# Kernel optimization log

Measured on AMD Instinct MI355X. Metric: run time of the kernel, lower is better.

## Reference

```python
import jax, jax.numpy as jnp
import numpy as np

H = 32
DECAY = 0.9


def setup_inputs() -> dict:
    key = jax.random.key(0)
    ks = jax.random.split(key, 6)
    B, T, D = 8, 4096, 1024
    x = jax.random.normal(ks[0], (B, T, D), dtype=jnp.float32)
    s = 1.0 / np.sqrt(D)
    Wv = jax.random.normal(ks[1], (D, D), dtype=jnp.float32) * s
    bv = jax.random.normal(ks[2], (D,), dtype=jnp.float32) * s
    Wo = jax.random.normal(ks[3], (D, D), dtype=jnp.float32) * s
    bo = jax.random.normal(ks[4], (D,), dtype=jnp.float32) * s
    w = jnp.asarray(DECAY ** np.arange(H), dtype=jnp.float32)
    decay_w = w / jnp.sum(w)
    return {"x": x, "Wv": Wv, "bv": bv, "Wo": Wo, "bo": bo, "decay_w": decay_w}


def reference(x, Wv, bv, Wo, bo, decay_w):
    # x: [B, T, D]. Original pads H zeros at front and unfolds windows of size H
    # with stride 1, producing T+1 windows: window t covers x[t-H .. t-1].
    # value_proj is linear and applied to every window copy, so it commutes with
    # the fixed-weight sum: attended = (sum_i w_i * x_window_i) @ Wv^T + bv*sum(w).
    B, T, D = x.shape
    Hlen = decay_w.shape[0]
    x_pad = jnp.pad(x, ((0, 0), (Hlen, 0), (0, 0)))  # [B, T+H, D]
    # Depthwise 1D conv over time with the (shared) decay kernel.
    kernel = jnp.broadcast_to(decay_w[:, None, None], (Hlen, 1, D))  # [W, I=1, O=D]
    s = jax.lax.conv_general_dilated(
        x_pad, kernel, window_strides=(1,), padding="VALID",
        dimension_numbers=("NWC", "WIO", "NWC"), feature_group_count=D,
    )  # [B, T+1, D]
    attended = s @ Wv.T + bv * jnp.sum(decay_w)
    return attended @ Wo.T + bo  # [B, T+1, D]
```

## Files before the change

### kernel.cpp

```cpp
#include <hip/hip_runtime.h>
#include <stdint.h>

#define D_DIM 1024
#define T_DIM 4096
#define B_DIM 8
#define M_REAL (B_DIM * (T_DIM + 1))
#define M_MAIN 32768
#define NWG 512

typedef short short8 __attribute__((ext_vector_type(8)));
typedef float floatx4 __attribute__((ext_vector_type(4)));

typedef const __attribute__((address_space(1))) void* gptr_t;
typedef __attribute__((address_space(3))) void* lptr_t;

__device__ __forceinline__ ushort f2bf(float f) {
  union { float f; uint32_t u; } v; v.f = f;
  uint32_t r = v.u + 0x7FFF + ((v.u >> 16) & 1);
  return (ushort)(r >> 16);
}
__device__ __forceinline__ float bf2f(ushort b) {
  union { uint32_t u; float f; } v; v.u = ((uint32_t)b) << 16; return v.f;
}

#define BARRIER()  asm volatile("s_barrier" ::: "memory")
#define WAIT_VM2() asm volatile("s_waitcnt vmcnt(2)" ::: "memory")
#define WAIT_VM0() asm volatile("s_waitcnt vmcnt(0)" ::: "memory")
#define WAIT_LGKM0() do { asm volatile("s_waitcnt lgkmcnt(0)" ::: "memory"); \
                          __builtin_amdgcn_sched_barrier(0); } while (0)
#define SP1() __builtin_amdgcn_s_setprio(1)
#define SP0() __builtin_amdgcn_s_setprio(0)

__global__ __launch_bounds__(1024) void gemm_w16_kernel(
    const ushort* __restrict__ A, const ushort* __restrict__ Bm,
    float* __restrict__ C, const float* __restrict__ bias)
{
  __shared__ char smem[65536];
  const int tid  = threadIdx.x;
  const int wave = tid >> 6;
  const int lane = tid & 63;
  const int wm = wave >> 2, wn = wave & 3;
  const int l15 = lane & 15, lhi = lane >> 4;

  const int bid = blockIdx.x;
  const int wg  = (bid & 7) * 64 + (bid >> 3);
  const int n0 = (wg & 3) * 256;
  const int m0 = (wg >> 2) * 256;

  const int srow = tid >> 2;
  const int ksw  = ((tid & 3) ^ ((tid >> 3) & 3)) * 8;
  const ushort* Aq = A  + (size_t)(m0 + srow) * D_DIM + ksw;
  const ushort* Bq = Bm + (size_t)(n0 + srow) * D_DIM + ksw;

  const int xorc = (lhi ^ ((l15 >> 1) & 3)) * 16;
  const int aoff = (wm * 64 + l15) * 64 + xorc;
  const int boff = (wn * 64 + l15) * 64 + xorc;

  short8 a[4], b[4];
  floatx4 acc[4][4] = {};

#define STAGE_W(PA, PB, S) do { \
  __builtin_amdgcn_global_load_lds((gptr_t)(PA), \
      (lptr_t)(smem + (S) * 16384 + wave * 1024), 16, 0, 0); \
  __builtin_amdgcn_global_load_lds((gptr_t)(PB), \
      (lptr_t)(smem + 32768 + (S) * 16384 + wave * 1024), 16, 0, 0); \
} while (0)

#define LDAB_W(S) do { \
  _Pragma("unroll") \
  for (int m = 0; m < 4; ++m) \
    a[m] = *(const short8*)(smem + (S) * 16384 + aoff + m * 1024); \
  _Pragma("unroll") \
  for (int n = 0; n < 4; ++n) \
    b[n] = *(const short8*)(smem + 32768 + (S) * 16384 + boff + n * 1024); \
} while (0)

#define MFMA_W() do { \
  _Pragma("unroll") \
  for (int m = 0; m < 4; ++m) \
    _Pragma("unroll") \
    for (int n = 0; n < 4; ++n) \
      acc[m][n] = __builtin_amdgcn_mfma_f32_16x16x32_bf16( \
          a[m], b[n], acc[m][n], 0, 0, 0); \
} while (0)

#define ITER_W(S0, STG, VMW) do { \
  if (STG) { STAGE_W(ApS, BpS, (S0) ^ 1); ApS += 32; BpS += 32; } \
  VMW; \
  BARRIER(); \
  LDAB_W(S0); \
  WAIT_LGKM0(); \
  SP1(); MFMA_W(); SP0(); \
  BARRIER(); \
} while (0)

  STAGE_W(Aq, Bq, 0);
  const ushort* ApS = Aq + 32;
  const ushort* BpS = Bq + 32;

#pragma unroll 1
  for (int it = 0; it < 15; ++it) {
    ITER_W(0, 1, WAIT_VM2());
    ITER_W(1, 1, WAIT_VM2());
  }
  ITER_W(0, 1, WAIT_VM2());
  ITER_W(1, 0, WAIT_VM0());

#pragma unroll
  for (int m = 0; m < 4; ++m)
#pragma unroll
    for (int n = 0; n < 4; ++n) {
      const int gn = n0 + wn * 64 + n * 16 + l15;
      const float bia = bias[gn];
#pragma unroll
      for (int j = 0; j < 4; ++j) {
        const int gm = m0 + wm * 64 + m * 16 + lhi * 4 + j;
        C[(size_t)gm * D_DIM + gn] = acc[m][n][j] + bia;
      }
    }
#undef STAGE_W
#undef LDAB_W
#undef MFMA_W
#undef ITER_W
}

__global__ __launch_bounds__(256) void tail_gemv_kernel(
    const ushort* __restrict__ S, const ushort* __restrict__ Wf,
    const float* __restrict__ cvec, float* __restrict__ out)
{
  const int wavei = threadIdx.x >> 6, lane = threadIdx.x & 63;
  const int c = blockIdx.x * 4 + wavei;
  float acc[8] = {};
  for (int i = 0; i < 16; ++i) {
    const int k = i * 64 + lane;
    const float wv = bf2f(Wf[(size_t)c * D_DIM + k]);
#pragma unroll
    for (int r = 0; r < 8; ++r)
      acc[r] += wv * bf2f(S[(size_t)(M_MAIN + r) * D_DIM + k]);
  }
#pragma unroll
  for (int r = 0; r < 8; ++r) {
#pragma unroll
    for (int off = 32; off; off >>= 1) acc[r] += __shfl_xor(acc[r], off, 64);
  }
  if (lane == 0) {
    const float bia = cvec[c];
#pragma unroll
    for (int r = 0; r < 8; ++r)
      out[(size_t)(M_MAIN + r) * D_DIM + c] = acc[r] + bia;
  }
}

__global__ __launch_bounds__(256) void gemm_bt_kernel(
    const ushort* __restrict__ A, const ushort* __restrict__ Bm,
    ushort* __restrict__ Cb, int K, int N)
{
  __shared__ ushort As[128][64];
  __shared__ ushort Bs[128][64];
  const int tid  = threadIdx.x;
  const int wave = tid >> 6;
  const int lane = tid & 63;
  const int wm = wave >> 1, wn = wave & 1;
  const int n0 = blockIdx.x * 128, m0 = blockIdx.y * 128;
  const int l15 = lane & 15, lhi = lane >> 4;

  floatx4 acc[4][4] = {};

  const int srow = tid >> 3;
  const int sk8  = (tid & 7) * 8;
  const ushort* Ab = A  + (size_t)(m0 + srow) * K + sk8;
  const ushort* Bb = Bm + (size_t)(n0 + srow) * K + sk8;

  for (int k0 = 0; k0 < K; k0 += 64) {
#pragma unroll
    for (int q = 0; q < 4; ++q)
      __builtin_amdgcn_global_load_lds((gptr_t)(Ab + k0 + (size_t)q * 32 * K),
          (lptr_t)((char*)&As[0][0] + (q * 256 + wave * 64) * 16), 16, 0, 0);
#pragma unroll
    for (int q = 0; q < 4; ++q)
      __builtin_amdgcn_global_load_lds((gptr_t)(Bb + k0 + (size_t)q * 32 * K),
          (lptr_t)((char*)&Bs[0][0] + (q * 256 + wave * 64) * 16), 16, 0, 0);
    __syncthreads();

#pragma unroll
    for (int kk = 0; kk < 2; ++kk) {
      short8 af[4], bfrg[4];
#pragma unroll
      for (int i = 0; i < 4; ++i) {
        af[i]   = *(const short8*)(&As[wm * 64 + i * 16 + l15][kk * 32 + lhi * 8]);
        bfrg[i] = *(const short8*)(&Bs[wn * 64 + i * 16 + l15][kk * 32 + lhi * 8]);
      }
#pragma unroll
      for (int mi = 0; mi < 4; ++mi)
#pragma unroll
        for (int ni = 0; ni < 4; ++ni)
          acc[mi][ni] = __builtin_amdgcn_mfma_f32_16x16x32_bf16(
              af[mi], bfrg[ni], acc[mi][ni], 0, 0, 0);
    }
    __syncthreads();
  }

#pragma unroll
  for (int mi = 0; mi < 4; ++mi)
#pragma unroll
    for (int ni = 0; ni < 4; ++ni) {
      const int gn = n0 + wn * 64 + ni * 16 + l15;
#pragma unroll
      for (int j = 0; j < 4; ++j) {
        const int gm = m0 + wm * 64 + mi * 16 + lhi * 4 + j;
        Cb[(size_t)gm * N + gn] = f2bf(acc[mi][ni][j]);
      }
    }
}

#define CTCH 256
__global__ __launch_bounds__(256) void conv_kernel(
    const float* __restrict__ x, const float* __restrict__ dw,
    ushort* __restrict__ S)
{
  const int b   = blockIdx.y;
  const int col = blockIdx.z * 256 + threadIdx.x;
  const int t0  = blockIdx.x * CTCH;

  float w[32];
#pragma unroll
  for (int i = 0; i < 32; ++i) w[i] = dw[i];
  const float rinv = w[0] / w[1];
  const float w31  = w[31];
  const float c0   = -w[0] * rinv;

  const float* xb = x + (size_t)b * T_DIM * D_DIM + col;
  ushort*      Sb = S + (size_t)b * (T_DIM + 1) * D_DIM + col;

  float prev[32], cur[32];
  float s;
  if (blockIdx.x == 0) {
#pragma unroll
    for (int i = 0; i < 32; ++i) prev[i] = 0.f;
    s = 0.f;
    Sb[0] = f2bf(0.f);
  } else {
#pragma unroll
    for (int i = 0; i < 32; ++i) prev[i] = xb[(size_t)(t0 - 32 + i) * D_DIM];
    s = 0.f;
#pragma unroll
    for (int i = 0; i < 32; ++i) s = __builtin_fmaf(w[i], prev[i], s);
  }

#pragma unroll 1
  for (int g = 0; g < 8; g += 2) {
#pragma unroll
    for (int i = 0; i < 32; ++i) cur[i] = xb[(size_t)(t0 + g * 32 + i) * D_DIM];
#pragma unroll
    for (int j = 0; j < 32; ++j) {
      s = __builtin_fmaf(s, rinv, __builtin_fmaf(prev[j], c0, w31 * cur[j]));
      Sb[(size_t)(t0 + g * 32 + 1 + j) * D_DIM] = f2bf(s);
    }
    s = 0.f;
#pragma unroll
    for (int i = 0; i < 32; ++i) s = __builtin_fmaf(w[i], cur[i], s);
#pragma unroll
    for (int i = 0; i < 32; ++i) prev[i] = xb[(size_t)(t0 + (g + 1) * 32 + i) * D_DIM];
#pragma unroll
    for (int j = 0; j < 32; ++j) {
      s = __builtin_fmaf(s, rinv, __builtin_fmaf(cur[j], c0, w31 * prev[j]));
      Sb[(size_t)(t0 + (g + 1) * 32 + 1 + j) * D_DIM] = f2bf(s);
    }
    s = 0.f;
#pragma unroll
    for (int i = 0; i < 32; ++i) s = __builtin_fmaf(w[i], prev[i], s);
  }
}

__global__ __launch_bounds__(256) void prep_kernel(
    const float* __restrict__ Wo, const float* __restrict__ Wv,
    const float* __restrict__ bv, const float* __restrict__ bo,
    const float* __restrict__ dw,
    ushort* __restrict__ WoB, ushort* __restrict__ WvT,
    float* __restrict__ cvec)
{
  __shared__ float tile[32][33];
  const int bid = blockIdx.x;
  const int tid = threadIdx.x;

  if (bid < 1024) {
    const int i = bid * 256 + tid;
    const float4 v = ((const float4*)Wo)[i];
    ushort4 o = make_ushort4(f2bf(v.x), f2bf(v.y), f2bf(v.z), f2bf(v.w));
    *(ushort4*)(WoB + (size_t)i * 4) = o;
  } else if (bid < 2048) {
    const int b2 = bid - 1024;
    const int c0 = (b2 & 31) * 32, r0 = (b2 >> 5) * 32;
    const int tx = tid & 31, ty = tid >> 5;
#pragma unroll
    for (int j = 0; j < 4; ++j)
      tile[ty + j * 8][tx] = Wv[(size_t)(r0 + ty + j * 8) * D_DIM + c0 + tx];
    __syncthreads();
#pragma unroll
    for (int j = 0; j < 4; ++j)
      WvT[(size_t)(c0 + ty + j * 8) * D_DIM + r0 + tx] = f2bf(tile[tx][ty + j * 8]);
  } else {
    const int j    = (bid - 2048) * 4 + (tid >> 6);
    const int lane = tid & 63;
    float sumw = 0.f;
#pragma unroll
    for (int i = 0; i < 32; ++i) sumw += dw[i];
    float s = 0.f;
    for (int k = lane; k < D_DIM; k += 64) s += Wo[(size_t)j * D_DIM + k] * bv[k];
#pragma unroll
    for (int off = 32; off; off >>= 1) s += __shfl_xor(s, off, 64);
    if (lane == 0) cvec[j] = sumw * s + bo[j];
  }
}

extern "C" void kernel_launch(void* const* d_in, const int* in_sizes, int n_in,
                              void* d_out, int out_size, void* d_ws, size_t ws_size,
                              hipStream_t stream) {
  const float* x  = (const float*)d_in[0];
  const float* Wv = (const float*)d_in[1];
  const float* bv = (const float*)d_in[2];
  const float* Wo = (const float*)d_in[3];
  const float* bo = (const float*)d_in[4];
  const float* dw = (const float*)d_in[5];
  float* out = (float*)d_out;

  char* ws = (char*)d_ws;
  ushort* S      = (ushort*)ws;
  ushort* WoB    = (ushort*)(ws + (size_t)M_REAL * D_DIM * 2);
  ushort* WvT    = WoB + (size_t)D_DIM * D_DIM;
  ushort* Wfused = WvT + (size_t)D_DIM * D_DIM;
  float*  cvec   = (float*)(Wfused + (size_t)D_DIM * D_DIM);

  prep_kernel<<<dim3(2304), dim3(256), 0, stream>>>(
      Wo, Wv, bv, bo, dw, WoB, WvT, cvec);

  gemm_bt_kernel<<<dim3(8, 8), dim3(256), 0, stream>>>(
      WoB, WvT, Wfused, D_DIM, D_DIM);

  conv_kernel<<<dim3(T_DIM / CTCH, B_DIM, 4), dim3(256), 0, stream>>>(x, dw, S);

  gemm_w16_kernel<<<dim3(NWG), dim3(1024), 0, stream>>>(S, Wfused, out, cvec);
  tail_gemv_kernel<<<dim3(256), dim3(256), 0, stream>>>(S, Wfused, cvec, out);
}
```

Before: 157.4 us.

## Merge conv with weight-fusion GEMM and tail GEMV into main GEMM launch

The conv kernel and the small Wo·Wv GEMM, which are independent, now run as one launch split by block index, so they can execute concurrently. The tail GEMV for the last 8 rows is folded into the main GEMM launch as 16 extra 1024-thread blocks that each handle 64 output columns. Together this cuts two kernel launches and lets small, underfilled kernels overlap with other work. In exchange the extra tail blocks may finish after the main GEMM tiles, and the conv branch now shares a kernel whose LDS footprint is sized for the GEMM branch.

Measured after the change: 173.7 us. 10.3% more time.

```diff
diff --git a/kernel.cpp b/kernel.cpp
--- a/kernel.cpp
+++ b/kernel.cpp
@@ -37,12 +37,42 @@
 {
   __shared__ char smem[65536];
   const int tid  = threadIdx.x;
+  const int bid  = blockIdx.x;
+
+  if (bid >= NWG) {
+    const int eb = bid - NWG;
+    const int wv = tid >> 6, lane = tid & 63;
+#pragma unroll 1
+    for (int cc = 0; cc < 4; ++cc) {
+      const int c = eb * 64 + wv * 4 + cc;
+      float a8[8] = {};
+      for (int i = 0; i < 16; ++i) {
+        const int k = i * 64 + lane;
+        const float wvv = bf2f(Bm[(size_t)c * D_DIM + k]);
+#pragma unroll
+        for (int r = 0; r < 8; ++r)
+          a8[r] += wvv * bf2f(A[(size_t)(M_MAIN + r) * D_DIM + k]);
+      }
+#pragma unroll
+      for (int r = 0; r < 8; ++r) {
+#pragma unroll
+        for (int off = 32; off; off >>= 1) a8[r] += __shfl_xor(a8[r], off, 64);
+      }
+      if (lane == 0) {
+        const float bia = bias[c];
+#pragma unroll
+        for (int r = 0; r < 8; ++r)
+          C[(size_t)(M_MAIN + r) * D_DIM + c] = a8[r] + bia;
+      }
+    }
+    return;
+  }
+
   const int wave = tid >> 6;
   const int lane = tid & 63;
   const int wm = wave >> 2, wn = wave & 3;
   const int l15 = lane & 15, lhi = lane >> 4;
 
-  const int bid = blockIdx.x;
   const int wg  = (bid & 7) * 64 + (bid >> 3);
   const int n0 = (wg & 3) * 256;
   const int m0 = (wg >> 2) * 256;
@@ -124,61 +154,96 @@
 #undef ITER_W
 }
 
-__global__ __launch_bounds__(256) void tail_gemv_kernel(
-    const ushort* __restrict__ S, const ushort* __restrict__ Wf,
-    const float* __restrict__ cvec, float* __restrict__ out)
-{
-  const int wavei = threadIdx.x >> 6, lane = threadIdx.x & 63;
-  const int c = blockIdx.x * 4 + wavei;
-  float acc[8] = {};
-  for (int i = 0; i < 16; ++i) {
-    const int k = i * 64 + lane;
-    const float wv = bf2f(Wf[(size_t)c * D_DIM + k]);
-#pragma unroll
-    for (int r = 0; r < 8; ++r)
-      acc[r] += wv * bf2f(S[(size_t)(M_MAIN + r) * D_DIM + k]);
-  }
-#pragma unroll
-  for (int r = 0; r < 8; ++r) {
-#pragma unroll
-    for (int off = 32; off; off >>= 1) acc[r] += __shfl_xor(acc[r], off, 64);
-  }
-  if (lane == 0) {
-    const float bia = cvec[c];
-#pragma unroll
-    for (int r = 0; r < 8; ++r)
-      out[(size_t)(M_MAIN + r) * D_DIM + c] = acc[r] + bia;
-  }
-}
-
-__global__ __launch_bounds__(256) void gemm_bt_kernel(
-    const ushort* __restrict__ A, const ushort* __restrict__ Bm,
-    ushort* __restrict__ Cb, int K, int N)
+#define CTCH 256
+__global__ __launch_bounds__(256) void conv_bt_kernel(
+    const float* __restrict__ x, const float* __restrict__ dw,
+    ushort* __restrict__ S,
+    const ushort* __restrict__ WoB, const ushort* __restrict__ WvT,
+    ushort* __restrict__ Wfused)
 {
   __shared__ ushort As[128][64];
   __shared__ ushort Bs[128][64];
-  const int tid  = threadIdx.x;
+  const int bid = blockIdx.x;
+  const int tid = threadIdx.x;
+
+  if (bid < 512) {
+    const int t0  = (bid & 15) * CTCH;
+    const int b   = (bid >> 4) & 7;
+    const int col = (bid >> 7) * 256 + tid;
+
+    float w[32];
+#pragma unroll
+    for (int i = 0; i < 32; ++i) w[i] = dw[i];
+    const float rinv = w[0] / w[1];
+    const float w31  = w[31];
+    const float c0   = -w[0] * rinv;
+
+    const float* xb = x + (size_t)b * T_DIM * D_DIM + col;
+    ushort*      Sb = S + (size_t)b * (T_DIM + 1) * D_DIM + col;
+
+    float prev[32], cur[32];
+    float s;
+    if ((bid & 15) == 0) {
+#pragma unroll
+      for (int i = 0; i < 32; ++i) prev[i] = 0.f;
+      s = 0.f;
+      Sb[0] = f2bf(0.f);
+    } else {
+#pragma unroll
+      for (int i = 0; i < 32; ++i) prev[i] = xb[(size_t)(t0 - 32 + i) * D_DIM];
+      s = 0.f;
+#pragma unroll
+      for (int i = 0; i < 32; ++i) s = __builtin_fmaf(w[i], prev[i], s);
+    }
+
+#pragma unroll 1
+    for (int g = 0; g < 8; g += 2) {
+#pragma unroll
+      for (int i = 0; i < 32; ++i) cur[i] = xb[(size_t)(t0 + g * 32 + i) * D_DIM];
+#pragma unroll
+      for (int j = 0; j < 32; ++j) {
+        s = __builtin_fmaf(s, rinv, __builtin_fmaf(prev[j], c0, w31 * cur[j]));
+        Sb[(size_t)(t0 + g * 32 + 1 + j) * D_DIM] = f2bf(s);
+      }
+      s = 0.f;
+#pragma unroll
+      for (int i = 0; i < 32; ++i) s = __builtin_fmaf(w[i], cur[i], s);
+#pragma unroll
+      for (int i = 0; i < 32; ++i) prev[i] = xb[(size_t)(t0 + (g + 1) * 32 + i) * D_DIM];
+#pragma unroll
+      for (int j = 0; j < 32; ++j) {
+        s = __builtin_fmaf(s, rinv, __builtin_fmaf(cur[j], c0, w31 * prev[j]));
+        Sb[(size_t)(t0 + (g + 1) * 32 + 1 + j) * D_DIM] = f2bf(s);
+      }
+      s = 0.f;
+#pragma unroll
+      for (int i = 0; i < 32; ++i) s = __builtin_fmaf(w[i], prev[i], s);
+    }
+    return;
+  }
+
+  const int bid2 = bid - 512;
   const int wave = tid >> 6;
   const int lane = tid & 63;
   const int wm = wave >> 1, wn = wave & 1;
-  const int n0 = blockIdx.x * 128, m0 = blockIdx.y * 128;
+  const int n0 = (bid2 & 7) * 128, m0 = (bid2 >> 3) * 128;
   const int l15 = lane & 15, lhi = lane >> 4;
 
   floatx4 acc[4][4] = {};
 
   const int srow = tid >> 3;
   const int sk8  = (tid & 7) * 8;
-  const ushort* Ab = A  + (size_t)(m0 + srow) * K + sk8;
-  const ushort* Bb = Bm + (size_t)(n0 + srow) * K + sk8;
-
-  for (int k0 = 0; k0 < K; k0 += 64) {
+  const ushort* Ab = WoB + (size_t)(m0 + srow) * D_DIM + sk8;
+  const ushort* Bb = WvT + (size_t)(n0 + srow) * D_DIM + sk8;
+
+  for (int k0 = 0; k0 < D_DIM; k0 += 64) {
 #pragma unroll
     for (int q = 0; q < 4; ++q)
-      __builtin_amdgcn_global_load_lds((gptr_t)(Ab + k0 + (size_t)q * 32 * K),
+      __builtin_amdgcn_global_load_lds((gptr_t)(Ab + k0 + (size_t)q * 32 * D_DIM),
           (lptr_t)((char*)&As[0][0] + (q * 256 + wave * 64) * 16), 16, 0, 0);
 #pragma unroll
     for (int q = 0; q < 4; ++q)
-      __builtin_amdgcn_global_load_lds((gptr_t)(Bb + k0 + (size_t)q * 32 * K),
+      __builtin_amdgcn_global_load_lds((gptr_t)(Bb + k0 + (size_t)q * 32 * D_DIM),
           (lptr_t)((char*)&Bs[0][0] + (q * 256 + wave * 64) * 16), 16, 0, 0);
     __syncthreads();
 
@@ -208,68 +273,9 @@
 #pragma unroll
       for (int j = 0; j < 4; ++j) {
         const int gm = m0 + wm * 64 + mi * 16 + lhi * 4 + j;
-        Cb[(size_t)gm * N + gn] = f2bf(acc[mi][ni][j]);
-      }
-    }
-}
-
-#define CTCH 256
-__global__ __launch_bounds__(256) void conv_kernel(
-    const float* __restrict__ x, const float* __restrict__ dw,
-    ushort* __restrict__ S)
-{
-  const int b   = blockIdx.y;
-  const int col = blockIdx.z * 256 + threadIdx.x;
-  const int t0  = blockIdx.x * CTCH;
-
-  float w[32];
-#pragma unroll
-  for (int i = 0; i < 32; ++i) w[i] = dw[i];
-  const float rinv = w[0] / w[1];
-  const float w31  = w[31];
-  const float c0   = -w[0] * rinv;
-
-  const float* xb = x + (size_t)b * T_DIM * D_DIM + col;
-  ushort*      Sb = S + (size_t)b * (T_DIM + 1) * D_DIM + col;
-
-  float prev[32], cur[32];
-  float s;
-  if (blockIdx.x == 0) {
-#pragma unroll
-    for (int i = 0; i < 32; ++i) prev[i] = 0.f;
-    s = 0.f;
-    Sb[0] = f2bf(0.f);
-  } else {
-#pragma unroll
-    for (int i = 0; i < 32; ++i) prev[i] = xb[(size_t)(t0 - 32 + i) * D_DIM];
-    s = 0.f;
-#pragma unroll
-    for (int i = 0; i < 32; ++i) s = __builtin_fmaf(w[i], prev[i], s);
-  }
-
-#pragma unroll 1
-  for (int g = 0; g < 8; g += 2) {
-#pragma unroll
-    for (int i = 0; i < 32; ++i) cur[i] = xb[(size_t)(t0 + g * 32 + i) * D_DIM];
-#pragma unroll
-    for (int j = 0; j < 32; ++j) {
-      s = __builtin_fmaf(s, rinv, __builtin_fmaf(prev[j], c0, w31 * cur[j]));
-      Sb[(size_t)(t0 + g * 32 + 1 + j) * D_DIM] = f2bf(s);
-    }
-    s = 0.f;
-#pragma unroll
-    for (int i = 0; i < 32; ++i) s = __builtin_fmaf(w[i], cur[i], s);
-#pragma unroll
-    for (int i = 0; i < 32; ++i) prev[i] = xb[(size_t)(t0 + (g + 1) * 32 + i) * D_DIM];
-#pragma unroll
-    for (int j = 0; j < 32; ++j) {
-      s = __builtin_fmaf(s, rinv, __builtin_fmaf(cur[j], c0, w31 * prev[j]));
-      Sb[(size_t)(t0 + (g + 1) * 32 + 1 + j) * D_DIM] = f2bf(s);
-    }
-    s = 0.f;
-#pragma unroll
-    for (int i = 0; i < 32; ++i) s = __builtin_fmaf(w[i], prev[i], s);
-  }
+        Wfused[(size_t)gm * D_DIM + gn] = f2bf(acc[mi][ni][j]);
+      }
+    }
 }
 
 __global__ __launch_bounds__(256) void prep_kernel(
@@ -334,11 +340,9 @@
   prep_kernel<<<dim3(2304), dim3(256), 0, stream>>>(
       Wo, Wv, bv, bo, dw, WoB, WvT, cvec);
 
-  gemm_bt_kernel<<<dim3(8, 8), dim3(256), 0, stream>>>(
-      WoB, WvT, Wfused, D_DIM, D_DIM);
-
-  conv_kernel<<<dim3(T_DIM / CTCH, B_DIM, 4), dim3(256), 0, stream>>>(x, dw, S);
-
-  gemm_w16_kernel<<<dim3(NWG), dim3(1024), 0, stream>>>(S, Wfused, out, cvec);
-  tail_gemv_kernel<<<dim3(256), dim3(256), 0, stream>>>(S, Wfused, cvec, out);
-}
+  conv_bt_kernel<<<dim3(576), dim3(256), 0, stream>>>(
+      x, dw, S, WoB, WvT, Wfused);
+
+  gemm_w16_kernel<<<dim3(NWG + 16), dim3(1024), 0, stream>>>(
+      S, Wfused, out, cvec);
+}
```
